# Performance work log

Measured on AMD Instinct MI355X. Metric: run time of the kernel, lower is better.

Reference implementation:

```python
import jax, jax.numpy as jnp
import numpy as np

D_MODEL = 2048
NUM_HEADS = 16
HEAD_DIM = D_MODEL // NUM_HEADS
B, T = 4, 2048


def setup_inputs() -> dict:
    key = jax.random.key(0)
    ks = jax.random.split(key, 9)
    s = 1.0 / np.sqrt(D_MODEL)
    inp = {"x": jax.random.normal(ks[0], (B, T, D_MODEL), dtype=jnp.float32)}
    for i, name in enumerate(["q", "k", "v", "o"]):
        inp[f"W{name}"] = jax.random.uniform(ks[1 + 2 * i], (D_MODEL, D_MODEL), minval=-s, maxval=s, dtype=jnp.float32)
        inp[f"b{name}"] = jax.random.uniform(ks[2 + 2 * i], (D_MODEL,), minval=-s, maxval=s, dtype=jnp.float32)
    return inp


def reference(x, Wq, bq, Wk, bk, Wv, bv, Wo, bo):
    Bx, Tx, _ = x.shape
    H, Dh = NUM_HEADS, HEAD_DIM
    # torch Linear: y = x @ W.T + b
    q = (x @ Wq.T + bq).reshape(Bx, Tx, H, Dh).transpose(0, 2, 1, 3)  # [B,H,T,D]
    k = (x @ Wk.T + bk).reshape(Bx, Tx, H, Dh).transpose(0, 2, 1, 3)
    v = (x @ Wv.T + bv).reshape(Bx, Tx, H, Dh).transpose(0, 2, 1, 3)
    scale = 1.0 / np.sqrt(Dh).astype(np.float32)
    scores = jnp.einsum('bhqd,bhkd->bhqk', q, k) * scale  # [B,H,T,T] (no causal mask, as in source)
    attn = jax.nn.softmax(scores, axis=-1)
    out = jnp.einsum('bhqk,bhkd->bhqd', attn, v)  # [B,H,T,D]
    out = out.transpose(0, 2, 1, 3).reshape(Bx, Tx, H * Dh)
    return out @ Wo.T + bo
```

## Files before the change

kernel.cpp:

```cpp
#include <hip/hip_runtime.h>
#include <hip/hip_bf16.h>

typedef __bf16 bf16x8 __attribute__((ext_vector_type(8)));
typedef __bf16 bf16x4 __attribute__((ext_vector_type(4)));
typedef float floatx4 __attribute__((ext_vector_type(4)));

#define MFMA16(a, b, c) __builtin_amdgcn_mfma_f32_16x16x32_bf16((a), (b), (c), 0, 0, 0)

#define GLOAD16(g, l) __builtin_amdgcn_global_load_lds( \
    (const __attribute__((address_space(1))) unsigned int*)(g), \
    (__attribute__((address_space(3))) unsigned int*)(l), 16, 0, 0)

static constexpr int DM = 2048, NH = 16, HD = 128, BATCH = 4, SEQ = 2048;
static constexpr int MROWS = BATCH * SEQ;
static constexpr float SCALE = 0.08838834764831845f;
static constexpr float PMAX = 3.0f;

static constexpr size_t XE = (size_t)MROWS * DM;
static constexpr size_t WE = (size_t)DM * DM;

__global__ __launch_bounds__(256) void cvt_all(
    const float* __restrict__ x, const float* __restrict__ Wq,
    const float* __restrict__ Wk, const float* __restrict__ Wv,
    const float* __restrict__ Wo, __bf16* __restrict__ dst) {
  const size_t total = XE + 4 * WE;
  size_t stride = (size_t)gridDim.x * 256 * 8;
  for (size_t i = ((size_t)blockIdx.x * 256 + threadIdx.x) * 8; i < total; i += stride) {
    const float* src;
    size_t off;
    if (i < XE) { src = x; off = i; }
    else {
      size_t j = i - XE;
      int seg = (int)(j / WE);
      off = j - (size_t)seg * WE;
      src = seg == 0 ? Wq : (seg == 1 ? Wk : (seg == 2 ? Wv : Wo));
    }
    float4 a = *reinterpret_cast<const float4*>(src + off);
    float4 b = *reinterpret_cast<const float4*>(src + off + 4);
    bf16x8 r;
    r[0] = (__bf16)a.x; r[1] = (__bf16)a.y; r[2] = (__bf16)a.z; r[3] = (__bf16)a.w;
    r[4] = (__bf16)b.x; r[5] = (__bf16)b.y; r[6] = (__bf16)b.z; r[7] = (__bf16)b.w;
    *reinterpret_cast<bf16x8*>(dst + i) = r;
  }
}

__device__ __forceinline__ void gemm256_core(
    const __bf16* __restrict__ A, const __bf16* __restrict__ W,
    unsigned short* sA, unsigned short* sB,
    int tm, int tn, floatx4 (&acc)[8][4]) {
  const int tid = threadIdx.x;
  const int wave = tid >> 6, lane = tid & 63;
  const int q = lane >> 4, ml = lane & 15;
  const int wm = wave >> 2, wn = wave & 3;

  const int csrc = (tid & 3) ^ ((tid >> 3) & 3);
  const __bf16* gA = A + (size_t)(tm + (tid >> 2)) * DM + csrc * 8;
  const __bf16* gB = W + (size_t)(tn + (tid >> 2)) * DM + csrc * 8;
  const size_t rstep = (size_t)128 * DM;
  const int ldsW = wave * 512;

  const int fsw = (q ^ ((ml >> 1) & 3)) * 8;
  const int aOff = (wm * 128 + ml) * 32 + fsw;
  const int bOff = (wn * 64 + ml) * 32 + fsw;

#define STAGE256(s_) do { \
    const int _r = ((s_) & 3) * 8192;   \
    const int _k = (s_) * 32;           \
    GLOAD16(gA + _k,         sA + _r + ldsW); \
    GLOAD16(gA + _k + rstep, sA + _r + 4096 + ldsW); \
    GLOAD16(gB + _k,         sB + _r + ldsW); \
    GLOAD16(gB + _k + rstep, sB + _r + 4096 + ldsW); \
  } while (0)

  STAGE256(0); STAGE256(1); STAGE256(2);
  asm volatile("s_waitcnt vmcnt(8)" ::: "memory");
  __builtin_amdgcn_s_barrier();

#pragma unroll 4
  for (int p = 0; p < 64; ++p) {
    const int regO = (p & 3) * 8192;
    bf16x8 aF[8], bF[4];
#pragma unroll
    for (int t = 0; t < 8; ++t)
      aF[t] = *reinterpret_cast<const bf16x8*>(sA + regO + aOff + t * 512);
#pragma unroll
    for (int t = 0; t < 4; ++t)
      bF[t] = *reinterpret_cast<const bf16x8*>(sB + regO + bOff + t * 512);

    STAGE256((p + 3) & 63);
    asm volatile("s_waitcnt vmcnt(8)" ::: "memory");
    __builtin_amdgcn_s_barrier();

    __builtin_amdgcn_s_setprio(1);
#pragma unroll
    for (int mt = 0; mt < 8; ++mt)
#pragma unroll
      for (int ct = 0; ct < 4; ++ct)
        acc[mt][ct] = MFMA16(aF[mt], bF[ct], acc[mt][ct]);
    __builtin_amdgcn_s_setprio(0);
    __builtin_amdgcn_s_barrier();
    asm volatile("" ::: "memory");
  }
#undef STAGE256
}

__global__ __launch_bounds__(512, 2) void qkv_gemm256(
    const __bf16* __restrict__ X,
    const __bf16* __restrict__ Wq, const __bf16* __restrict__ Wk,
    const __bf16* __restrict__ Wv,
    const float* __restrict__ bq, const float* __restrict__ bk,
    const float* __restrict__ bv,
    __bf16* __restrict__ qh, __bf16* __restrict__ kh, __bf16* __restrict__ vt) {
  __shared__ unsigned short sA[4 * 256 * 32];
  __shared__ unsigned short sB[4 * 256 * 32];
  const int bx = blockIdx.x;
  const int which = bx >> 3;
  const int tn = (bx & 7) * 256;
  const int tm = blockIdx.y * 256;
  const __bf16* W = which == 0 ? Wq : (which == 1 ? Wk : Wv);
  const float* bias = which == 0 ? bq : (which == 1 ? bk : bv);

  floatx4 acc[8][4] = {};
  gemm256_core(X, W, sA, sB, tm, tn, acc);

  const int tid = threadIdx.x, wave = tid >> 6, lane = tid & 63;
  const int q = lane >> 4, ml = lane & 15;
  const int wm = wave >> 2, wn = wave & 3;
#pragma unroll
  for (int ct = 0; ct < 4; ++ct) {
    int n = tn + wn * 64 + ct * 16 + ml;
    float bv_ = bias[n];
    int h = n >> 7, d = n & 127;
#pragma unroll
    for (int mt = 0; mt < 8; ++mt) {
      int m0 = tm + wm * 128 + mt * 16 + q * 4;
      int b = m0 >> 11, t = m0 & 2047;
      if (which < 2) {
        __bf16* dst = which == 0 ? qh : kh;
#pragma unroll
        for (int r = 0; r < 4; ++r)
          dst[((size_t)(b * 16 + h) * SEQ + t + r) * HD + d] = (__bf16)(acc[mt][ct][r] + bv_);
      } else {
        bf16x4 pk;
#pragma unroll
        for (int r = 0; r < 4; ++r) pk[r] = (__bf16)(acc[mt][ct][r] + bv_);
        *reinterpret_cast<bf16x4*>(vt + (size_t)((b * 16 + h) * 128 + d) * SEQ + t) = pk;
      }
    }
  }
}

__global__ __launch_bounds__(512, 2) void proj_gemm256(
    const __bf16* __restrict__ A, const __bf16* __restrict__ W,
    const float* __restrict__ bias, float* __restrict__ out) {
  __shared__ unsigned short sA[4 * 256 * 32];
  __shared__ unsigned short sB[4 * 256 * 32];
  const int tn = blockIdx.x * 256;
  const int tm = blockIdx.y * 256;

  floatx4 acc[8][4] = {};
  gemm256_core(A, W, sA, sB, tm, tn, acc);

  const int tid = threadIdx.x, wave = tid >> 6, lane = tid & 63;
  const int q = lane >> 4, ml = lane & 15;
  const int wm = wave >> 2, wn = wave & 3;
#pragma unroll
  for (int ct = 0; ct < 4; ++ct) {
    int n = tn + wn * 64 + ct * 16 + ml;
    float bv_ = bias[n];
#pragma unroll
    for (int mt = 0; mt < 8; ++mt) {
      int m0 = tm + wm * 128 + mt * 16 + q * 4;
#pragma unroll
      for (int r = 0; r < 4; ++r)
        out[(size_t)(m0 + r) * DM + n] = acc[mt][ct][r] + bv_;
    }
  }
}

__global__ __launch_bounds__(512) void mha_attn(
    const __bf16* __restrict__ Q, const __bf16* __restrict__ Kg,
    const __bf16* __restrict__ Vt, __bf16* __restrict__ O) {
  __shared__ unsigned short sK[64 * 128];
  __shared__ unsigned short sV[128 * 64];
  __shared__ unsigned short sP[128 * 72];

  const int tid = threadIdx.x;
  const int bh = blockIdx.x;
  const int t0 = blockIdx.y * 128;
  const int wave = tid >> 6, lane = tid & 63;
  const int q = lane >> 4, ml = lane & 15;
  const int wrow = wave * 16;

  bf16x8 qf[4];
  {
    const __bf16* qrow = Q + ((size_t)bh * SEQ + t0 + wrow + ml) * HD;
#pragma unroll
    for (int s = 0; s < 4; ++s)
      qf[s] = *reinterpret_cast<const bf16x8*>(qrow + s * 32 + q * 8);
  }

  floatx4 oacc[8] = {};
  float lsum[4] = {0.f, 0.f, 0.f, 0.f};

  const __bf16* kbase = Kg + (size_t)bh * SEQ * HD;
  const __bf16* vbase = Vt + (size_t)bh * HD * SEQ;
  const int lrow4 = lane >> 4, c16 = lane & 15;
  const int lrow8 = lane >> 3, c8 = lane & 7;

  for (int kt = 0; kt < SEQ / 64; ++kt) {
    const int key0 = kt * 64;
    __syncthreads();
#pragma unroll
    for (int i = 0; i < 2; ++i) {
      int kr0 = wave * 8 + i * 4;
      int kc = c16 ^ ((i * 4 + lrow4) & 7);
      GLOAD16(kbase + (size_t)(key0 + kr0 + lrow4) * HD + kc * 8, &sK[kr0 * 128]);
      int vr0 = wave * 16 + i * 8;
      int vc = c8 ^ (lrow8 & 7);
      GLOAD16(vbase + (size_t)(vr0 + lrow8) * SEQ + key0 + vc * 8, &sV[vr0 * 64]);
    }
    __syncthreads();

    floatx4 sacc[4] = {};
#pragma unroll
    for (int s = 0; s < 4; ++s) {
#pragma unroll
      for (int ct = 0; ct < 4; ++ct) {
        bf16x8 kf = *reinterpret_cast<const bf16x8*>(
            &sK[(ct * 16 + ml) * 128 + (((s * 4 + q) ^ (ml & 7)) * 8)]);
        sacc[ct] = MFMA16(qf[s], kf, sacc[ct]);
      }
    }

#pragma unroll
    for (int ct = 0; ct < 4; ++ct) {
#pragma unroll
      for (int r = 0; r < 4; ++r) {
        float p = __expf(fmaf(sacc[ct][r], SCALE, -PMAX));
        sacc[ct][r] = p;
        lsum[r] += p;
        __bf16 pb = (__bf16)p;
        sP[(wrow + q * 4 + r) * 72 + ct * 16 + ml] = __builtin_bit_cast(unsigned short, pb);
      }
    }

#pragma unroll
    for (int s = 0; s < 2; ++s) {
      bf16x8 pf = *reinterpret_cast<const bf16x8*>(&sP[(wrow + ml) * 72 + s * 32 + q * 8]);
#pragma unroll
      for (int ot = 0; ot < 8; ++ot) {
        bf16x8 vf = *reinterpret_cast<const bf16x8*>(
            &sV[(ot * 16 + ml) * 64 + (((s * 4 + q) ^ (ml & 7)) * 8)]);
        oacc[ot] = MFMA16(pf, vf, oacc[ot]);
      }
    }
  }

#pragma unroll
  for (int r = 0; r < 4; ++r) {
    float s = lsum[r];
    s += __shfl_xor(s, 1); s += __shfl_xor(s, 2);
    s += __shfl_xor(s, 4); s += __shfl_xor(s, 8);
    lsum[r] = 1.0f / s;
  }
  const int b = bh >> 4, h = bh & 15;
  __bf16* obase = O + ((size_t)b * SEQ + t0 + wrow) * DM + h * HD;
#pragma unroll
  for (int ot = 0; ot < 8; ++ot) {
    int d = ot * 16 + ml;
#pragma unroll
    for (int r = 0; r < 4; ++r)
      obase[(size_t)(q * 4 + r) * DM + d] = (__bf16)(oacc[ot][r] * lsum[r]);
  }
}

__device__ inline bf16x8 ld8s(const float* p) {
  float4 a = *reinterpret_cast<const float4*>(p);
  float4 b = *reinterpret_cast<const float4*>(p + 4);
  bf16x8 r;
  r[0] = (__bf16)a.x; r[1] = (__bf16)a.y; r[2] = (__bf16)a.z; r[3] = (__bf16)a.w;
  r[4] = (__bf16)b.x; r[5] = (__bf16)b.y; r[6] = (__bf16)b.z; r[7] = (__bf16)b.w;
  return r;
}
__device__ inline bf16x8 ld8s(const __bf16* p) {
  int4 v = *reinterpret_cast<const int4*>(p);
  return __builtin_bit_cast(bf16x8, v);
}

template <typename TA>
__global__ __launch_bounds__(256) void gemm_slow(
    const TA* __restrict__ A, const float* __restrict__ W,
    const float* __restrict__ bias, void* __restrict__ C, int mode, int out_f32) {
  __shared__ unsigned short sA[128 * 72];
  __shared__ unsigned short sW[128 * 72];
  const int tid = threadIdx.x;
  const int tn = blockIdx.x * 128, tm = blockIdx.y * 128;
  const int wave = tid >> 6, lane = tid & 63;
  const int q = lane >> 4, ml = lane & 15;
  const int waveM = (wave >> 1) * 64, waveN = (wave & 1) * 64;
  const int srow = tid >> 3, sc8 = tid & 7;
  floatx4 acc[4][4] = {};
  for (int k0 = 0; k0 < DM; k0 += 64) {
    bf16x8 va[4], vb[4];
#pragma unroll
    for (int i = 0; i < 4; ++i) {
      int row = srow + 32 * i;
      va[i] = ld8s(A + (size_t)(tm + row) * DM + k0 + sc8 * 8);
      vb[i] = ld8s(W + (size_t)(tn + row) * DM + k0 + sc8 * 8);
    }
    __syncthreads();
#pragma unroll
    for (int i = 0; i < 4; ++i) {
      int row = srow + 32 * i;
      *reinterpret_cast<int4*>(&sA[row * 72 + sc8 * 8]) = __builtin_bit_cast(int4, va[i]);
      *reinterpret_cast<int4*>(&sW[row * 72 + sc8 * 8]) = __builtin_bit_cast(int4, vb[i]);
    }
    __syncthreads();
#pragma unroll
    for (int s = 0; s < 2; ++s) {
      bf16x8 aF[4], bF[4];
#pragma unroll
      for (int t = 0; t < 4; ++t)
        aF[t] = *reinterpret_cast<const bf16x8*>(&sA[(waveM + t * 16 + ml) * 72 + s * 32 + q * 8]);
#pragma unroll
      for (int t = 0; t < 4; ++t)
        bF[t] = *reinterpret_cast<const bf16x8*>(&sW[(waveN + t * 16 + ml) * 72 + s * 32 + q * 8]);
#pragma unroll
      for (int rt = 0; rt < 4; ++rt)
#pragma unroll
        for (int ct = 0; ct < 4; ++ct)
          acc[rt][ct] = MFMA16(aF[rt], bF[ct], acc[rt][ct]);
    }
  }
#pragma unroll
  for (int ct = 0; ct < 4; ++ct) {
    int n = tn + waveN + ct * 16 + ml;
    float bv = bias[n];
    int h = n >> 7, d = n & 127;
#pragma unroll
    for (int rt = 0; rt < 4; ++rt) {
      int m0 = tm + waveM + rt * 16 + q * 4;
      int b = m0 >> 11, t = m0 & 2047;
      if (mode == 0) {
        if (out_f32) {
#pragma unroll
          for (int r = 0; r < 4; ++r)
            ((float*)C)[(size_t)(m0 + r) * DM + n] = acc[rt][ct][r] + bv;
        } else {
#pragma unroll
          for (int r = 0; r < 4; ++r)
            ((__bf16*)C)[(size_t)(m0 + r) * DM + n] = (__bf16)(acc[rt][ct][r] + bv);
        }
      } else if (mode == 1) {
        bf16x4 pk;
#pragma unroll
        for (int r = 0; r < 4; ++r) pk[r] = (__bf16)(acc[rt][ct][r] + bv);
        *reinterpret_cast<bf16x4*>((__bf16*)C + (size_t)((b * 16 + h) * 128 + d) * SEQ + t) = pk;
      } else {
#pragma unroll
        for (int r = 0; r < 4; ++r)
          ((__bf16*)C)[((size_t)(b * 16 + h) * SEQ + t + r) * HD + d] =
              (__bf16)(acc[rt][ct][r] + bv);
      }
    }
  }
}

extern "C" void kernel_launch(void* const* d_in, const int* in_sizes, int n_in,
                              void* d_out, int out_size, void* d_ws, size_t ws_size,
                              hipStream_t stream) {
  const float* x  = (const float*)d_in[0];
  const float* Wq = (const float*)d_in[1]; const float* bq = (const float*)d_in[2];
  const float* Wk = (const float*)d_in[3]; const float* bk = (const float*)d_in[4];
  const float* Wv = (const float*)d_in[5]; const float* bv = (const float*)d_in[6];
  const float* Wo = (const float*)d_in[7]; const float* bo = (const float*)d_in[8];

  const size_t needA = 64 + 2 * (4 * XE + 4 * WE);
  dim3 gq(24, 32), gp(8, 32), gs(16, 64), ga(BATCH * NH, SEQ / 128);

  if (ws_size >= needA + 256) {
    __bf16* xc  = (__bf16*)((char*)d_ws + 64);
    __bf16* Wqc = xc + XE;
    __bf16* Wkc = Wqc + WE;
    __bf16* Wvc = Wkc + WE;
    __bf16* Woc = Wvc + WE;
    __bf16* qh  = Woc + WE;
    __bf16* kh  = qh + XE;
    __bf16* vt  = kh + XE;
    __bf16* aw  = xc;

    cvt_all<<<4096, 256, 0, stream>>>(x, Wq, Wk, Wv, Wo, xc);
    qkv_gemm256<<<gq, 512, 0, stream>>>(xc, Wqc, Wkc, Wvc, bq, bk, bv, qh, kh, vt);
    mha_attn<<<ga, 512, 0, stream>>>(qh, kh, vt, aw);
    proj_gemm256<<<gp, 512, 0, stream>>>(aw, Woc, bo, (float*)d_out);
  } else {
    __bf16* qh = (__bf16*)((char*)d_ws + 64);
    __bf16* kh = qh + XE;
    __bf16* vt = kh + XE;
    __bf16* aw = vt + XE;
    gemm_slow<float><<<gs, 256, 0, stream>>>(x, Wq, bq, qh, 2, 0);
    gemm_slow<float><<<gs, 256, 0, stream>>>(x, Wk, bk, kh, 2, 0);
    gemm_slow<float><<<gs, 256, 0, stream>>>(x, Wv, bv, vt, 1, 0);
    mha_attn<<<ga, 512, 0, stream>>>(qh, kh, vt, aw);
    gemm_slow<__bf16><<<gs, 256, 0, stream>>>(aw, Wo, bo, d_out, 0, 1);
  }
}
```

Baseline: 656.1 us.

## Restructure GEMM pipeline with deeper prefetch and stage Q/K epilogue through LDS

The GEMM main loop now issues the next stage's global-to-LDS loads before waiting. It waits with a looser vmcnt so more loads stay in flight, and the last iterations are peeled so no wrapped-around redundant loads are issued. A sched_barrier pins instruction ordering. The Q/K epilogue now writes bias-added bf16 results into swizzled LDS tiles and then emits 16-byte coalesced global stores, replacing scattered 2-byte stores. This adds an extra LDS round trip and a block-wide sync in the epilogue.

New measurement: 626.6 us. 4.5% less time.

```diff
diff --git a/kernel.cpp b/kernel.cpp
--- a/kernel.cpp
+++ b/kernel.cpp
@@ -72,35 +72,38 @@
     GLOAD16(gB + _k + rstep, sB + _r + 4096 + ldsW); \
   } while (0)
 
+#define GPHASE(p_, vm_, stage_) do { \
+    if (stage_) STAGE256((p_) + 3); \
+    asm volatile("s_waitcnt vmcnt(%0)" :: "i"(vm_) : "memory"); \
+    __builtin_amdgcn_s_barrier(); \
+    __builtin_amdgcn_sched_barrier(0); \
+    const int regO = ((p_) & 3) * 8192; \
+    bf16x8 aF[8], bF[4]; \
+    _Pragma("unroll") \
+    for (int t = 0; t < 4; ++t) \
+      bF[t] = *reinterpret_cast<const bf16x8*>(sB + regO + bOff + t * 512); \
+    _Pragma("unroll") \
+    for (int t = 0; t < 8; ++t) \
+      aF[t] = *reinterpret_cast<const bf16x8*>(sA + regO + aOff + t * 512); \
+    __builtin_amdgcn_s_setprio(1); \
+    _Pragma("unroll") \
+    for (int mt = 0; mt < 8; ++mt) \
+      _Pragma("unroll") \
+      for (int ct = 0; ct < 4; ++ct) \
+        acc[mt][ct] = MFMA16(aF[mt], bF[ct], acc[mt][ct]); \
+    __builtin_amdgcn_s_setprio(0); \
+    __builtin_amdgcn_s_barrier(); \
+  } while (0)
+
   STAGE256(0); STAGE256(1); STAGE256(2);
-  asm volatile("s_waitcnt vmcnt(8)" ::: "memory");
-  __builtin_amdgcn_s_barrier();
 
 #pragma unroll 4
-  for (int p = 0; p < 64; ++p) {
-    const int regO = (p & 3) * 8192;
-    bf16x8 aF[8], bF[4];
-#pragma unroll
-    for (int t = 0; t < 8; ++t)
-      aF[t] = *reinterpret_cast<const bf16x8*>(sA + regO + aOff + t * 512);
-#pragma unroll
-    for (int t = 0; t < 4; ++t)
-      bF[t] = *reinterpret_cast<const bf16x8*>(sB + regO + bOff + t * 512);
-
-    STAGE256((p + 3) & 63);
-    asm volatile("s_waitcnt vmcnt(8)" ::: "memory");
-    __builtin_amdgcn_s_barrier();
-
-    __builtin_amdgcn_s_setprio(1);
-#pragma unroll
-    for (int mt = 0; mt < 8; ++mt)
-#pragma unroll
-      for (int ct = 0; ct < 4; ++ct)
-        acc[mt][ct] = MFMA16(aF[mt], bF[ct], acc[mt][ct]);
-    __builtin_amdgcn_s_setprio(0);
-    __builtin_amdgcn_s_barrier();
-    asm volatile("" ::: "memory");
-  }
+  for (int p = 0; p < 60; ++p) GPHASE(p, 12, 1);
+  GPHASE(60, 12, 1);
+  GPHASE(61, 8, 0);
+  GPHASE(62, 4, 0);
+  GPHASE(63, 0, 0);
+#undef GPHASE
 #undef STAGE256
 }
 
@@ -126,21 +129,48 @@
   const int tid = threadIdx.x, wave = tid >> 6, lane = tid & 63;
   const int q = lane >> 4, ml = lane & 15;
   const int wm = wave >> 2, wn = wave & 3;
-#pragma unroll
-  for (int ct = 0; ct < 4; ++ct) {
-    int n = tn + wn * 64 + ct * 16 + ml;
-    float bv_ = bias[n];
-    int h = n >> 7, d = n & 127;
-#pragma unroll
-    for (int mt = 0; mt < 8; ++mt) {
-      int m0 = tm + wm * 128 + mt * 16 + q * 4;
-      int b = m0 >> 11, t = m0 & 2047;
-      if (which < 2) {
-        __bf16* dst = which == 0 ? qh : kh;
-#pragma unroll
-        for (int r = 0; r < 4; ++r)
-          dst[((size_t)(b * 16 + h) * SEQ + t + r) * HD + d] = (__bf16)(acc[mt][ct][r] + bv_);
-      } else {
+
+  __syncthreads();
+
+  if (which < 2) {
+    unsigned short* reg = (wave < 4) ? sA + wave * 8192 : sB + (wave - 4) * 8192;
+#pragma unroll
+    for (int ct = 0; ct < 4; ++ct) {
+      int n = tn + wn * 64 + ct * 16 + ml;
+      float bv_ = bias[n];
+#pragma unroll
+      for (int mt = 0; mt < 8; ++mt)
+#pragma unroll
+        for (int r = 0; r < 4; ++r) {
+          int row = mt * 16 + q * 4 + r;
+          int col = ct * 16 + ml;
+          __bf16 pb = (__bf16)(acc[mt][ct][r] + bv_);
+          reg[row * 64 + (((col >> 3) ^ ((row >> 1) & 7)) << 3) + (col & 7)] =
+              __builtin_bit_cast(unsigned short, pb);
+        }
+    }
+    __bf16* dst = which == 0 ? qh : kh;
+    const int rr = lane >> 3, cc = lane & 7;
+#pragma unroll
+    for (int i = 0; i < 16; ++i) {
+      int row = i * 8 + rr;
+      int4 v = *reinterpret_cast<const int4*>(
+          reg + row * 64 + ((cc ^ ((row >> 1) & 7)) << 3));
+      int m = tm + wm * 128 + row;
+      int n0 = tn + wn * 64 + cc * 8;
+      int b = m >> 11, t = m & 2047, h = n0 >> 7, d = n0 & 127;
+      *reinterpret_cast<int4*>(dst + ((size_t)(b * 16 + h) * SEQ + t) * HD + d) = v;
+    }
+  } else {
+#pragma unroll
+    for (int ct = 0; ct < 4; ++ct) {
+      int n = tn + wn * 64 + ct * 16 + ml;
+      float bv_ = bias[n];
+      int h = n >> 7, d = n & 127;
+#pragma unroll
+      for (int mt = 0; mt < 8; ++mt) {
+        int m0 = tm + wm * 128 + mt * 16 + q * 4;
+        int b = m0 >> 11, t = m0 & 2047;
         bf16x4 pk;
 #pragma unroll
         for (int r = 0; r < 4; ++r) pk[r] = (__bf16)(acc[mt][ct][r] + bv_);
```
